# Optimization experiments

Measured on AMD Instinct MI355X. Metric: run time of the kernel, lower is better.

Reference implementation:

```python
import jax, jax.numpy as jnp
import numpy as np

N, L, E, CE = 16384, 50, 64, 128
N_USERS, N_RATINGS, N_CONTENTS = 100000, 6, 50000

def _lin(key, din, dout):
    k1, k2 = jax.random.split(key)
    s = 1.0 / np.sqrt(din)
    return (jax.random.uniform(k1, (din, dout), jnp.float32, -s, s),
            jax.random.uniform(k2, (dout,), jnp.float32, -s, s))

def setup_inputs() -> dict:
    key = jax.random.key(0)
    ks = jax.random.split(key, 16)
    We_w, We_b = _lin(ks[0], CE, E)
    W1_w, W1_b = _lin(ks[1], 2 * E, E)
    W2_w, W2_b = _lin(ks[2], E, E)
    A1_w, A1_b = _lin(ks[3], 2 * E, E)
    A2_w, A2_b = _lin(ks[4], E, E)
    A3_w, A3_b = _lin(ks[5], E, 1)
    Ow_w, Ow_b = _lin(ks[6], 2 * E, E)
    return {
        "u2e": jax.random.normal(ks[7], (N_USERS, E), jnp.float32),
        "r2e": jax.random.normal(ks[8], (N_RATINGS, E), jnp.float32),
        "content_emb": jax.random.normal(ks[9], (N_CONTENTS, CE), jnp.float32),
        "We_w": We_w, "We_b": We_b,
        "W1_w": W1_w, "W1_b": W1_b,
        "W2_w": W2_w, "W2_b": W2_b,
        "A1_w": A1_w, "A1_b": A1_b,
        "A2_w": A2_w, "A2_b": A2_b,
        "A3_w": A3_w, "A3_b": A3_b,
        "Ow_w": Ow_w, "Ow_b": Ow_b,
        "nodes": jnp.arange(N, dtype=jnp.int64) if jax.config.jax_enable_x64 else jnp.arange(N, dtype=jnp.int32),
        "pu_history": jax.random.randint(ks[10], (N, L), 0, N_USERS),
        "pr_history": jax.random.randint(ks[11], (N, L), 0, N_RATINGS),
        "lengths": jax.random.randint(ks[12], (N,), 1, L + 1),
        "pr_content": jax.random.randint(ks[13], (N,), 0, N_CONTENTS),
    }

def reference(u2e, r2e, content_emb, We_w, We_b, W1_w, W1_b, W2_w, W2_b,
              A1_w, A1_b, A2_w, A2_b, A3_w, A3_b, Ow_w, Ow_b,
              nodes, pu_history, pr_history, lengths, pr_content):
    # mask of valid (non-padded) neighbors per node: [N, L]
    mask = jnp.arange(pu_history.shape[1])[None, :] < lengths[:, None]
    # post content representation: [N, E]
    post = jax.nn.relu(content_emb[pr_content] @ We_w + We_b)
    # neighbor embeddings: [N, L, E]
    u = u2e[pu_history]
    r = r2e[pr_history]
    x = jax.nn.relu(jnp.concatenate([u, r], axis=-1) @ W1_w + W1_b)
    o = jax.nn.relu(x @ W2_w + W2_b)  # [N, L, E]
    # attention over variable-length neighbor history
    pr = jnp.broadcast_to(post[:, None, :], o.shape)
    a = jax.nn.relu(jnp.concatenate([o, pr], axis=-1) @ A1_w + A1_b)
    a = jax.nn.relu(a @ A2_w + A2_b)
    logits = (a @ A3_w + A3_b)[..., 0]  # [N, L]
    logits = jnp.where(mask, logits, -jnp.inf)
    att = jax.nn.softmax(logits, axis=1)  # [N, L], padded slots -> 0
    hist = jnp.einsum("nl,nle->ne", att, o)  # [N, E]
    out = jax.nn.relu(jnp.concatenate([hist, post], axis=-1) @ Ow_w + Ow_b)
    return out
```

## Files before the change

### kernel.cpp

```cpp
#include <hip/hip_runtime.h>
#include <hip/hip_bf16.h>
#include <math.h>


#define NN 16384
#define LL 50
#define EE 64
#define NUE 6400000

typedef __attribute__((ext_vector_type(8))) short short8;
typedef __attribute__((ext_vector_type(4))) float f32x4;

#define LGKM_BAR() asm volatile("s_waitcnt lgkmcnt(0)\n\ts_barrier" ::: "memory")

static __device__ __forceinline__ unsigned short f2bf(float x) {
  __hip_bfloat16 h = __float2bfloat16(x);
  unsigned short u;
  __builtin_memcpy(&u, &h, 2);
  return u;
}

static __device__ __forceinline__ float bf2f(unsigned short u) {
  unsigned int v = ((unsigned int)u) << 16;
  float f;
  __builtin_memcpy(&f, &v, 4);
  return f;
}

static __device__ __forceinline__ f32x4 ld4(const float* p) {
  return *(const f32x4*)p;
}

static __device__ __forceinline__ f32x4 relu4(f32x4 a) {
  f32x4 r;
  r[0] = fmaxf(a[0], 0.f); r[1] = fmaxf(a[1], 0.f);
  r[2] = fmaxf(a[2], 0.f); r[3] = fmaxf(a[3], 0.f);
  return r;
}

static __device__ __forceinline__ void gl_lds16(const unsigned short* g,
                                                unsigned char* l) {
  __builtin_amdgcn_global_load_lds(
      (const __attribute__((address_space(1))) void*)g,
      (__attribute__((address_space(3))) void*)l, 16, 0, 0);
}

#define MFMA(A, B, C) __builtin_amdgcn_mfma_f32_16x16x32_bf16((A), (B), (C), 0, 0, 0)
#define SWZ(row, byteoff) ((byteoff) ^ (((row) & 7) << 4))

__global__ __launch_bounds__(1024)
void pre_kernel(const float* __restrict__ u2e, const float* __restrict__ r2e,
                const float* __restrict__ content_emb,
                const int* __restrict__ pr_content,
                const float* __restrict__ We_w, const float* __restrict__ We_b,
                const float* __restrict__ W1_w, const float* __restrict__ W2_w,
                const float* __restrict__ A1_w, const float* __restrict__ A1_b,
                const float* __restrict__ A2_w,
                const int* __restrict__ lengths,
                unsigned short* __restrict__ ur_bf,
                int* __restrict__ buckets, int* __restrict__ wdesc,
                int* __restrict__ Wout, unsigned short* __restrict__ frag_ws,
                float* __restrict__ post_ws, float* __restrict__ abase_ws) {
  const int b = blockIdx.x;
  const int tid = (int)threadIdx.x;
  __shared__ float ce_s[16][128];
  __shared__ float post_s[16][64];
  __shared__ int cnt_s[4];

  if (b == 0) {
    const int lanei = tid & 63;
    if (tid < 4) cnt_s[tid] = 0;
    __syncthreads();
    for (int i0 = 0; i0 < NN; i0 += 1024) {
      const int n = i0 + tid;
      const int ln = lengths[n];
      const int nt = (ln + 15) >> 4;
      const int entry = n | (ln << 14);
#pragma unroll
      for (int bb = 1; bb <= 4; ++bb) {
        const unsigned long long mask = __ballot(nt == bb);
        if (mask) {
          const int leader = __ffsll((long long)mask) - 1;
          int base = 0;
          if (lanei == leader)
            base = atomicAdd(&cnt_s[bb - 1], (int)__popcll(mask));
          base = __shfl(base, leader);
          if (nt == bb) {
            const int rank = __popcll(mask & ((1ull << lanei) - 1ull));
            buckets[(bb - 1) * NN + base + rank] = entry;
          }
        }
      }
    }
    __syncthreads();

    const int c1 = cnt_s[0], c2 = cnt_s[1], c3 = cnt_s[2], c4 = cnt_s[3];
    const int u1 = (c1 < c3) ? c1 : c3;
    const int p2 = c2 >> 1, odd2 = c2 & 1;
    const int rem1 = c1 - u1;
    const int o2ones = odd2 ? ((rem1 < 2) ? rem1 : 2) : 0;
    const int rem1b = rem1 - o2ones;
    const int w4 = c4, w3 = c3, w2 = p2 + odd2, w1 = (rem1b + 3) >> 2;
    const int W = w4 + w3 + w2 + w1;
    if (tid == 0) *Wout = W;

    const int* b1 = buckets;
    const int* b2 = buckets + NN;
    const int* b3 = buckets + 2 * NN;
    const int* b4 = buckets + 3 * NN;
#define ENC(e, t) (((e) & 0x3FFF) | ((t) << 14) | (((e) >> 14) << 16))
    for (int w = tid; w < W; w += 1024) {
      int d0 = -1, d1 = -1, d2 = -1, d3 = -1;
      if (w < w4) {
        const int e = b4[w];
        d0 = ENC(e, 0); d1 = ENC(e, 1); d2 = ENC(e, 2); d3 = ENC(e, 3);
      } else if (w < w4 + w3) {
        const int i = w - w4;
        const int e = b3[i];
        d0 = ENC(e, 0); d1 = ENC(e, 1); d2 = ENC(e, 2);
        if (i < u1) d3 = ENC(b1[i], 0);
      } else if (w < w4 + w3 + w2) {
        const int i = w - w4 - w3;
        if (i < p2) {
          const int ea = b2[2 * i], eb = b2[2 * i + 1];
          d0 = ENC(ea, 0); d1 = ENC(ea, 1); d2 = ENC(eb, 0); d3 = ENC(eb, 1);
        } else {
          const int ea = b2[c2 - 1];
          d0 = ENC(ea, 0); d1 = ENC(ea, 1);
          if (o2ones > 0) d2 = ENC(b1[u1], 0);
          if (o2ones > 1) d3 = ENC(b1[u1 + 1], 0);
        }
      } else {
        const int i = w - w4 - w3 - w2;
        const int basei = u1 + o2ones + 4 * i;
        if (basei + 0 < c1) d0 = ENC(b1[basei + 0], 0);
        if (basei + 1 < c1) d1 = ENC(b1[basei + 1], 0);
        if (basei + 2 < c1) d2 = ENC(b1[basei + 2], 0);
        if (basei + 3 < c1) d3 = ENC(b1[basei + 3], 0);
      }
      int4 v; v.x = d0; v.y = d1; v.z = d2; v.w = d3;
      *(int4*)(wdesc + 4 * w) = v;
    }
#undef ENC
  } else if (b < 1025) {
    const int total8 = (NUE + 384) / 8;
    for (int i = (b - 1) * 1024 + tid; i < total8; i += 1024 * 1024) {
      const long long e0 = (long long)i * 8;
      const float* src = (e0 < NUE) ? (u2e + e0) : (r2e + (e0 - NUE));
      float4 a = *(const float4*)src;
      float4 bb = *(const float4*)(src + 4);
      short8 v;
      v[0] = (short)f2bf(a.x); v[1] = (short)f2bf(a.y);
      v[2] = (short)f2bf(a.z); v[3] = (short)f2bf(a.w);
      v[4] = (short)f2bf(bb.x); v[5] = (short)f2bf(bb.y);
      v[6] = (short)f2bf(bb.z); v[7] = (short)f2bf(bb.w);
      *reinterpret_cast<short8*>(ur_bf + e0) = v;
    }
  } else if (b < 2049) {
    const int sub = tid >> 6;
    const int e = tid & 63;
    const int n = (b - 1025) * 16 + sub;
    const float* ce = content_emb + (size_t)pr_content[n] * 128;
    ce_s[sub][e] = ce[e];
    ce_s[sub][64 + e] = ce[64 + e];
    __syncthreads();
    float acc = We_b[e];
#pragma unroll 8
    for (int k = 0; k < 128; ++k)
      acc = fmaf(ce_s[sub][k], We_w[k * EE + e], acc);
    float po = fmaxf(acc, 0.f);
    post_s[sub][e] = po;
    post_ws[(size_t)n * EE + e] = po;
    __syncthreads();
    float ab = A1_b[e];
#pragma unroll 8
    for (int k = 0; k < 64; ++k)
      ab = fmaf(post_s[sub][k], A1_w[(64 + k) * EE + e], ab);
    abase_ws[(size_t)n * EE + e] = ab;
  } else {
    const int idx = (b - 2049) * 1024 + tid;
    if (idx < 2560) {
      const float* Wm;
      int w, s, lane;
      if (idx < 1024) {
        w = idx >> 8; s = (idx >> 6) & 3; lane = idx & 63; Wm = W1_w;
      } else {
        int r = idx - 1024;
        int li = r >> 9;
        w = (r >> 7) & 3; s = (r >> 6) & 1; lane = r & 63;
        Wm = (li == 0) ? W2_w : (li == 1) ? A1_w : A2_w;
      }
      const int g = lane >> 4, c = lane & 15;
#pragma unroll
      for (int j = 0; j < 8; ++j)
        frag_ws[idx * 8 + j] = f2bf(Wm[(32 * s + 8 * g + j) * EE + 16 * w + c]);
    }
  }
}

__global__
__attribute__((amdgpu_flat_work_group_size(256, 256)))
__attribute__((amdgpu_waves_per_eu(4, 4)))
void fused_kernel(const unsigned short* __restrict__ ur_bf,
                  const float* __restrict__ W1_b, const float* __restrict__ W2_b,
                  const float* __restrict__ A2_b,
                  const float* __restrict__ A3_w, const float* __restrict__ A3_b,
                  const float* __restrict__ Ow_w, const float* __restrict__ Ow_b,
                  const int* __restrict__ pu_history,
                  const int* __restrict__ pr_history,
                  const short8* __restrict__ pf,
                  const float* __restrict__ post_ws,
                  const float* __restrict__ abase_ws,
                  const int* __restrict__ wdesc, const int* __restrict__ Wptr,
                  float* __restrict__ out) {
  const int tid = (int)threadIdx.x;
  const int lane = tid & 63;
  const int w = tid >> 6;
  const int g = lane >> 4;
  const int c = lane & 15;

  __shared__ __align__(16) unsigned char xb0[16384];
  __shared__ __align__(16) unsigned char xb1[8192];
  __shared__ __align__(16) unsigned char xb2[8192];
  __shared__ float bias_s[256];
  __shared__ float lpart[4][64];
  __shared__ float att_s[64];
  __shared__ float h_s[4][128];

  short8 Wf1[4], Wf2[2], Wf3[2], Wf4[2];
#pragma unroll
  for (int s = 0; s < 4; ++s) Wf1[s] = pf[(w * 4 + s) * 64 + lane];
#pragma unroll
  for (int s = 0; s < 2; ++s) {
    Wf2[s] = pf[1024 + (w * 2 + s) * 64 + lane];
    Wf3[s] = pf[1536 + (w * 2 + s) * 64 + lane];
    Wf4[s] = pf[2048 + (w * 2 + s) * 64 + lane];
  }
  if (tid < 64) {
    bias_s[tid]       = W1_b[tid];
    bias_s[64 + tid]  = W2_b[tid];
    bias_s[128 + tid] = A2_b[tid];
    bias_s[192 + tid] = A3_w[tid];
  }

  const float b3 = A3_b[0];
  const float owb = Ow_b[lane];
  const unsigned short* rbase = ur_bf + NUE;
  const int Wtot = *Wptr;
  const int stride = gridDim.x;

  const int r0 = lane >> 4;
  const int cE = (lane & 15) ^ r0;
  const int cO = (lane & 15) ^ (r0 + 4);
  const unsigned short* tabE = ((cE < 8) ? ur_bf : rbase) + (cE & 7) * 8;
  const unsigned short* tabO = ((cO < 8) ? ur_bf : rbase) + (cO & 7) * 8;
  const int* histE = (cE < 8) ? pu_history : pr_history;
  const int* histO = (cO < 8) ? pu_history : pr_history;
  unsigned char* const sbase = xb0 + w * 4096;

  if (blockIdx.x < Wtot) {
    const int dn = wdesc[blockIdx.x * 4 + w];
    if (dn >= 0) {
      const int nd = (dn & 0x3FFF) * LL + (((dn >> 14) & 3) << 4);
      const int lim = ((dn >> 16) & 63) - (((dn >> 14) & 3) << 4);
#pragma unroll
      for (int b = 0; b < 4; ++b) {
        const int row = b * 4 + r0;
        const int* hh = (b & 1) ? histO : histE;
        const unsigned short* tt = (b & 1) ? tabO : tabE;
        if (row < lim) {
          const int idx = hh[nd + row];
          gl_lds16(tt + (size_t)idx * EE, sbase + b * 1024);
        }
      }
    }
  }
  __syncthreads();

  for (int wi = blockIdx.x; wi < Wtot; wi += stride) {
    const int d0 = wdesc[wi * 4 + 0];
    const int d1 = wdesc[wi * 4 + 1];
    const int d2 = wdesc[wi * 4 + 2];
    const int d3 = wdesc[wi * 4 + 3];
    const int dw = (w == 0) ? d0 : (w == 1) ? d1 : (w == 2) ? d2 : d3;
    const bool fin = (dw >= 0) && (((dw >> 14) & 3) == 0);
    const int fnode = dw & 0x3FFF;
    const int flen = (dw >> 16) & 63;

    float po = 0.f;
    if (fin) po = post_ws[(size_t)fnode * EE + lane];

    const int win = wi + stride;
    int sidx0 = 0, sidx1 = 0, sidx2 = 0, sidx3 = 0;
    int svmask = 0;
    if (win < Wtot) {
      const int dn = wdesc[win * 4 + w];
      if (dn >= 0) {
        const int nd = (dn & 0x3FFF) * LL + (((dn >> 14) & 3) << 4);
        const int lim = ((dn >> 16) & 63) - (((dn >> 14) & 3) << 4);
        if (r0 + 0  < lim) { sidx0 = histE[nd + r0];      svmask |= 1; }
        if (r0 + 4  < lim) { sidx1 = histO[nd + r0 + 4];  svmask |= 2; }
        if (r0 + 8  < lim) { sidx2 = histE[nd + r0 + 8];  svmask |= 4; }
        if (r0 + 12 < lim) { sidx3 = histO[nd + r0 + 12]; svmask |= 8; }
      }
    }

    f32x4 acc[4];

    {
      const f32x4 binit = ld4(bias_s + 16 * w + 4 * g);
#pragma unroll
      for (int rt = 0; rt < 4; ++rt) acc[rt] = binit;
#pragma unroll
      for (int s = 0; s < 4; ++s)
#pragma unroll
        for (int rt = 0; rt < 4; ++rt) {
          const int row = rt * 16 + c;
          const short8 bf =
              *(const short8*)(xb0 + SWZ(row, row * 256 + s * 64 + g * 16));
          acc[rt] = MFMA(Wf1[s], bf, acc[rt]);
        }
#pragma unroll
      for (int rt = 0; rt < 4; ++rt) {
        const f32x4 v = relu4(acc[rt]);
        ushort4 p;
        p.x = f2bf(v[0]); p.y = f2bf(v[1]); p.z = f2bf(v[2]); p.w = f2bf(v[3]);
        const int row = rt * 16 + c;
        *(ushort4*)(xb1 + SWZ(row, row * 128 + w * 32 + g * 8)) = p;
      }
    }
    LGKM_BAR();

    if (svmask & 1) gl_lds16(tabE + (size_t)sidx0 * EE, sbase);
    if (svmask & 2) gl_lds16(tabO + (size_t)sidx1 * EE, sbase + 1024);
    if (svmask & 4) gl_lds16(tabE + (size_t)sidx2 * EE, sbase + 2048);
    if (svmask & 8) gl_lds16(tabO + (size_t)sidx3 * EE, sbase + 3072);

    {
      const f32x4 binit = ld4(bias_s + 64 + 16 * w + 4 * g);
#pragma unroll
      for (int rt = 0; rt < 4; ++rt) acc[rt] = binit;
#pragma unroll
      for (int s = 0; s < 2; ++s)
#pragma unroll
        for (int rt = 0; rt < 4; ++rt) {
          const int row = rt * 16 + c;
          const short8 bf =
              *(const short8*)(xb1 + SWZ(row, row * 128 + s * 64 + g * 16));
          acc[rt] = MFMA(Wf2[s], bf, acc[rt]);
        }
#pragma unroll
      for (int rt = 0; rt < 4; ++rt) {
        const f32x4 v = relu4(acc[rt]);
        ushort4 p;
        p.x = f2bf(v[0]); p.y = f2bf(v[1]); p.z = f2bf(v[2]); p.w = f2bf(v[3]);
        const int row = rt * 16 + c;
        *(ushort4*)(xb2 + SWZ(row, row * 128 + w * 32 + g * 8)) = p;
      }
    }
    LGKM_BAR();

    {
      {
        const int n0 = (d0 >= 0) ? (d0 & 0x3FFF) : 0;
        const int n1 = (d1 >= 0) ? (d1 & 0x3FFF) : 0;
        const int n2 = (d2 >= 0) ? (d2 & 0x3FFF) : 0;
        const int n3 = (d3 >= 0) ? (d3 & 0x3FFF) : 0;
        acc[0] = ld4(abase_ws + (size_t)n0 * EE + 16 * w + 4 * g);
        acc[1] = ld4(abase_ws + (size_t)n1 * EE + 16 * w + 4 * g);
        acc[2] = ld4(abase_ws + (size_t)n2 * EE + 16 * w + 4 * g);
        acc[3] = ld4(abase_ws + (size_t)n3 * EE + 16 * w + 4 * g);
      }
#pragma unroll
      for (int s = 0; s < 2; ++s)
#pragma unroll
        for (int rt = 0; rt < 4; ++rt) {
          const int row = rt * 16 + c;
          const short8 bf =
              *(const short8*)(xb2 + SWZ(row, row * 128 + s * 64 + g * 16));
          acc[rt] = MFMA(Wf3[s], bf, acc[rt]);
        }
#pragma unroll
      for (int rt = 0; rt < 4; ++rt) {
        const f32x4 v = relu4(acc[rt]);
        ushort4 p;
        p.x = f2bf(v[0]); p.y = f2bf(v[1]); p.z = f2bf(v[2]); p.w = f2bf(v[3]);
        const int row = rt * 16 + c;
        *(ushort4*)(xb1 + SWZ(row, row * 128 + w * 32 + g * 8)) = p;
      }
    }
    LGKM_BAR();

    {
      const f32x4 binit = ld4(bias_s + 128 + 16 * w + 4 * g);
#pragma unroll
      for (int rt = 0; rt < 4; ++rt) acc[rt] = binit;
#pragma unroll
      for (int s = 0; s < 2; ++s)
#pragma unroll
        for (int rt = 0; rt < 4; ++rt) {
          const int row = rt * 16 + c;
          const short8 bf =
              *(const short8*)(xb1 + SWZ(row, row * 128 + s * 64 + g * 16));
          acc[rt] = MFMA(Wf4[s], bf, acc[rt]);
        }
      const f32x4 a3 = ld4(bias_s + 192 + 16 * w + 4 * g);
#pragma unroll
      for (int rt = 0; rt < 4; ++rt) {
        const f32x4 r = relu4(acc[rt]);
        float p = r[0] * a3[0];
        p = fmaf(r[1], a3[1], p);
        p = fmaf(r[2], a3[2], p);
        p = fmaf(r[3], a3[3], p);
        p += __shfl_xor(p, 16);
        p += __shfl_xor(p, 32);
        if (lane < 16) lpart[w][rt * 16 + lane] = p;
      }
    }
    __syncthreads();

    if (fin) {
      const bool vr = (lane < flen);
      float lg = -INFINITY;
      if (vr) {
        const int row = w * 16 + lane;
        lg = lpart[0][row] + lpart[1][row] + lpart[2][row] + lpart[3][row] + b3;
      }
      float mx = lg;
#pragma unroll
      for (int off = 32; off > 0; off >>= 1)
        mx = fmaxf(mx, __shfl_xor(mx, off));
      const float e = __expf(lg - mx);
      float sm = e;
#pragma unroll
      for (int off = 32; off > 0; off >>= 1) sm += __shfl_xor(sm, off);
      if (vr) att_s[w * 16 + lane] = e / sm;

      float h0 = 0.f, h1 = 0.f;
      for (int r2 = 0; r2 + 1 < flen; r2 += 2) {
        const int ra = w * 16 + r2, rb = ra + 1;
        const unsigned short oa =
            *(const unsigned short*)(xb2 + SWZ(ra, ra * 128 + lane * 2));
        const unsigned short ob =
            *(const unsigned short*)(xb2 + SWZ(rb, rb * 128 + lane * 2));
        h0 = fmaf(att_s[ra], bf2f(oa), h0);
        h1 = fmaf(att_s[rb], bf2f(ob), h1);
      }
      if (flen & 1) {
        const int ra = w * 16 + flen - 1;
        const unsigned short oa =
            *(const unsigned short*)(xb2 + SWZ(ra, ra * 128 + lane * 2));
        h0 = fmaf(att_s[ra], bf2f(oa), h0);
      }
      h_s[w][lane] = h0 + h1;
      h_s[w][64 + lane] = po;

      float s0 = 0.f, s1 = 0.f, s2 = 0.f, s3 = 0.f;
#pragma unroll 8
      for (int k = 0; k < 128; k += 4) {
        s0 = fmaf(h_s[w][k],     Ow_w[(k)     * EE + lane], s0);
        s1 = fmaf(h_s[w][k + 1], Ow_w[(k + 1) * EE + lane], s1);
        s2 = fmaf(h_s[w][k + 2], Ow_w[(k + 2) * EE + lane], s2);
        s3 = fmaf(h_s[w][k + 3], Ow_w[(k + 3) * EE + lane], s3);
      }
      const float a = owb + ((s0 + s1) + (s2 + s3));
      out[(size_t)fnode * EE + lane] = fmaxf(a, 0.f);
    }
  }
}

template <int K>
__device__ __forceinline__ void mm2(const float* row0, const float* row1,
                                    const float* __restrict__ W, int e,
                                    float& acc0, float& acc1) {
  const float4* r0 = (const float4*)row0;
  const float4* r1 = (const float4*)row1;
#pragma unroll 4
  for (int k4 = 0; k4 < K / 4; ++k4) {
    float4 va = r0[k4];
    float4 vb = r1[k4];
    const float* w = W + (k4 * 4) * EE + e;
    float w0 = w[0], w1 = w[EE], w2 = w[2 * EE], w3 = w[3 * EE];
    acc0 = fmaf(va.x, w0, acc0);  acc1 = fmaf(vb.x, w0, acc1);
    acc0 = fmaf(va.y, w1, acc0);  acc1 = fmaf(vb.y, w1, acc1);
    acc0 = fmaf(va.z, w2, acc0);  acc1 = fmaf(vb.z, w2, acc1);
    acc0 = fmaf(va.w, w3, acc0);  acc1 = fmaf(vb.w, w3, acc1);
  }
}

__global__ __launch_bounds__(256, 4)
void postenc_kernel(
    const float* __restrict__ u2e, const float* __restrict__ r2e,
    const float* __restrict__ content_emb,
    const float* __restrict__ We_w, const float* __restrict__ We_b,
    const float* __restrict__ W1_w, const float* __restrict__ W1_b,
    const float* __restrict__ W2_w, const float* __restrict__ W2_b,
    const float* __restrict__ A1_w, const float* __restrict__ A1_b,
    const float* __restrict__ A2_w, const float* __restrict__ A2_b,
    const float* __restrict__ A3_w, const float* __restrict__ A3_b,
    const float* __restrict__ Ow_w, const float* __restrict__ Ow_b,
    const int* __restrict__ pu_history, const int* __restrict__ pr_history,
    const int* __restrict__ lengths, const int* __restrict__ pr_content,
    float* __restrict__ out) {
  const int n = blockIdx.x;
  const int tid = (int)threadIdx.x;
  const int e = tid & 63;
  const int g = tid >> 6;

  __shared__ float post_s[EE];
  __shared__ float abase_s[EE];
  __shared__ float in_s[8][128];
  __shared__ float x_s[8][EE];
  __shared__ float a_s[8][EE];
  __shared__ float o_s[56][EE];
  __shared__ float logit_s[EE];
  __shared__ float att_s[EE];
  __shared__ float red_s[4][EE];

  const int len = lengths[n];
  float p = 0.f;

  if (g == 0) {
    const float* ce = content_emb + (size_t)pr_content[n] * 128;
    float acc = We_b[e];
#pragma unroll 4
    for (int k = 0; k < 128; ++k) acc = fmaf(ce[k], We_w[k * EE + e], acc);
    p = fmaxf(acc, 0.f);
    post_s[e] = p;
    float ab = A1_b[e];
#pragma unroll
    for (int k = 0; k < 64; ++k) {
      float pk = __shfl(p, k);
      ab = fmaf(pk, A1_w[(64 + k) * EE + e], ab);
    }
    abase_s[e] = ab;
    logit_s[e] = -INFINITY;
  }
  __syncthreads();

  for (int lb = 0; lb < 56; lb += 8) {
    const int l0 = lb + g;
    const int l1 = l0 + 4;
    const bool v0 = l0 < LL;
    const bool v1 = l1 < LL;

    int pu0 = 0, pr0 = 0, pu1 = 0, pr1 = 0;
    if (v0) { pu0 = pu_history[n * LL + l0]; pr0 = pr_history[n * LL + l0]; }
    if (v1) { pu1 = pu_history[n * LL + l1]; pr1 = pr_history[n * LL + l1]; }
    in_s[g][e]          = v0 ? u2e[(size_t)pu0 * EE + e] : 0.f;
    in_s[g][64 + e]     = v0 ? r2e[pr0 * EE + e]         : 0.f;
    in_s[g + 4][e]      = v1 ? u2e[(size_t)pu1 * EE + e] : 0.f;
    in_s[g + 4][64 + e] = v1 ? r2e[pr1 * EE + e]         : 0.f;
    __syncthreads();

    float acc0 = W1_b[e], acc1 = acc0;
    mm2<128>(in_s[g], in_s[g + 4], W1_w, e, acc0, acc1);
    x_s[g][e]     = fmaxf(acc0, 0.f);
    x_s[g + 4][e] = fmaxf(acc1, 0.f);
    __syncthreads();

    acc0 = W2_b[e]; acc1 = acc0;
    mm2<64>(x_s[g], x_s[g + 4], W2_w, e, acc0, acc1);
    float o0 = fmaxf(acc0, 0.f);
    float o1 = fmaxf(acc1, 0.f);
    if (v0) o_s[l0][e] = o0;
    if (v1) o_s[l1][e] = o1;
    x_s[g][e]     = o0;
    x_s[g + 4][e] = o1;
    __syncthreads();

    acc0 = abase_s[e]; acc1 = acc0;
    mm2<64>(x_s[g], x_s[g + 4], A1_w, e, acc0, acc1);
    a_s[g][e]     = fmaxf(acc0, 0.f);
    a_s[g + 4][e] = fmaxf(acc1, 0.f);
    __syncthreads();

    acc0 = A2_b[e]; acc1 = acc0;
    mm2<64>(a_s[g], a_s[g + 4], A2_w, e, acc0, acc1);
    float w3 = A3_w[e];
    float p0 = fmaxf(acc0, 0.f) * w3;
    float p1 = fmaxf(acc1, 0.f) * w3;
#pragma unroll
    for (int off = 32; off > 0; off >>= 1) {
      p0 += __shfl_xor(p0, off);
      p1 += __shfl_xor(p1, off);
    }
    if (e == 0) {
      float b3 = A3_b[0];
      if (l0 < len) logit_s[l0] = p0 + b3;
      if (l1 < len) logit_s[l1] = p1 + b3;
    }
    __syncthreads();
  }

  if (g == 0) {
    float lg = logit_s[e];
    float m = lg;
#pragma unroll
    for (int off = 32; off > 0; off >>= 1) m = fmaxf(m, __shfl_xor(m, off));
    float pe = __expf(lg - m);
    float sm = pe;
#pragma unroll
    for (int off = 32; off > 0; off >>= 1) sm += __shfl_xor(sm, off);
    att_s[e] = pe / sm;
  }
  __syncthreads();

  {
    const int l_lo = 13 * g;
    const int l_hi = (13 * g + 13 < LL) ? 13 * g + 13 : LL;
    float h = 0.f;
    for (int l = l_lo; l < l_hi; ++l) h = fmaf(att_s[l], o_s[l][e], h);
    red_s[g][e] = h;
  }
  __syncthreads();

  if (g == 0) {
    float h = red_s[0][e] + red_s[1][e] + red_s[2][e] + red_s[3][e];
    float acc = Ow_b[e];
#pragma unroll
    for (int k = 0; k < 64; ++k) {
      float hk = __shfl(h, k);
      acc = fmaf(hk, Ow_w[k * EE + e], acc);
    }
#pragma unroll
    for (int k = 0; k < 64; ++k) {
      float pk = __shfl(p, k);
      acc = fmaf(pk, Ow_w[(64 + k) * EE + e], acc);
    }
    out[(size_t)n * EE + e] = fmaxf(acc, 0.f);
  }
}

extern "C" void kernel_launch(void* const* d_in, const int* in_sizes, int n_in,
                              void* d_out, int out_size, void* d_ws, size_t ws_size,
                              hipStream_t stream) {
  const float* u2e         = (const float*)d_in[0];
  const float* r2e         = (const float*)d_in[1];
  const float* content_emb = (const float*)d_in[2];
  const float* We_w = (const float*)d_in[3];
  const float* We_b = (const float*)d_in[4];
  const float* W1_w = (const float*)d_in[5];
  const float* W1_b = (const float*)d_in[6];
  const float* W2_w = (const float*)d_in[7];
  const float* W2_b = (const float*)d_in[8];
  const float* A1_w = (const float*)d_in[9];
  const float* A1_b = (const float*)d_in[10];
  const float* A2_w = (const float*)d_in[11];
  const float* A2_b = (const float*)d_in[12];
  const float* A3_w = (const float*)d_in[13];
  const float* A3_b = (const float*)d_in[14];
  const float* Ow_w = (const float*)d_in[15];
  const float* Ow_b = (const float*)d_in[16];
  const int* pu_history = (const int*)d_in[18];
  const int* pr_history = (const int*)d_in[19];
  const int* lengths    = (const int*)d_in[20];
  const int* pr_content = (const int*)d_in[21];
  float* out = (float*)d_out;

  const size_t FR_OFF  = 0;
  const size_t PO_OFF  = 65536;
  const size_t AB_OFF  = PO_OFF + (size_t)NN * EE * 4;
  const size_t UBF_OFF = AB_OFF + (size_t)NN * EE * 4;
  const size_t CNT_OFF = UBF_OFF + (size_t)(NUE + 384) * 2;
  const size_t BK_OFF  = CNT_OFF + 256;
  const size_t WD_OFF  = BK_OFF + (size_t)4 * NN * 4;
  const size_t NEED    = WD_OFF + (size_t)NN * 4 * 4;

  if (ws_size < NEED) {
    postenc_kernel<<<NN, 256, 0, stream>>>(
        u2e, r2e, content_emb, We_w, We_b, W1_w, W1_b, W2_w, W2_b,
        A1_w, A1_b, A2_w, A2_b, A3_w, A3_b, Ow_w, Ow_b,
        pu_history, pr_history, lengths, pr_content, out);
    return;
  }

  char* wsp = (char*)d_ws;
  unsigned short* frag_ws = (unsigned short*)(wsp + FR_OFF);
  float* post_ws  = (float*)(wsp + PO_OFF);
  float* abase_ws = (float*)(wsp + AB_OFF);
  unsigned short* ur_bf = (unsigned short*)(wsp + UBF_OFF);
  int* Wout_ws = (int*)(wsp + CNT_OFF);
  int* bk_ws   = (int*)(wsp + BK_OFF);
  int* wd_ws   = (int*)(wsp + WD_OFF);

  pre_kernel<<<2052, 1024, 0, stream>>>(
      u2e, r2e, content_emb, pr_content, We_w, We_b, W1_w, W2_w,
      A1_w, A1_b, A2_w, lengths, ur_bf, bk_ws, wd_ws, Wout_ws,
      frag_ws, post_ws, abase_ws);
  fused_kernel<<<1024, 256, 0, stream>>>(
      ur_bf, W1_b, W2_b, A2_b, A3_w, A3_b, Ow_w, Ow_b,
      pu_history, pr_history, (const short8*)frag_ws,
      post_ws, abase_ws, wd_ws, Wout_ws, out);
}
```

Measured before the change: 132.0 us.

## Replace static grid-stride work distribution with atomic work-stealing counter

New measurement: 163.4 us. 1.24x slower.

```diff
diff --git a/kernel.cpp b/kernel.cpp
--- a/kernel.cpp
+++ b/kernel.cpp
@@ -7,6 +7,7 @@
 #define LL 50
 #define EE 64
 #define NUE 6400000
+#define FGRID 1024
 
 typedef __attribute__((ext_vector_type(8))) short short8;
 typedef __attribute__((ext_vector_type(4))) float f32x4;
@@ -59,7 +60,8 @@
                 const int* __restrict__ lengths,
                 unsigned short* __restrict__ ur_bf,
                 int* __restrict__ buckets, int* __restrict__ wdesc,
-                int* __restrict__ Wout, unsigned short* __restrict__ frag_ws,
+                int* __restrict__ Wout, int* __restrict__ wctr,
+                unsigned short* __restrict__ frag_ws,
                 float* __restrict__ post_ws, float* __restrict__ abase_ws) {
   const int b = blockIdx.x;
   const int tid = (int)threadIdx.x;
@@ -70,6 +72,7 @@
   if (b == 0) {
     const int lanei = tid & 63;
     if (tid < 4) cnt_s[tid] = 0;
+    if (tid == 8) *wctr = FGRID;
     __syncthreads();
     for (int i0 = 0; i0 < NN; i0 += 1024) {
       const int n = i0 + tid;
@@ -212,6 +215,7 @@
                   const float* __restrict__ post_ws,
                   const float* __restrict__ abase_ws,
                   const int* __restrict__ wdesc, const int* __restrict__ Wptr,
+                  int* __restrict__ wctr,
                   float* __restrict__ out) {
   const int tid = (int)threadIdx.x;
   const int lane = tid & 63;
@@ -226,6 +230,7 @@
   __shared__ float lpart[4][64];
   __shared__ float att_s[64];
   __shared__ float h_s[4][128];
+  __shared__ int nxt_s;
 
   short8 Wf1[4], Wf2[2], Wf3[2], Wf4[2];
 #pragma unroll
@@ -247,7 +252,6 @@
   const float owb = Ow_b[lane];
   const unsigned short* rbase = ur_bf + NUE;
   const int Wtot = *Wptr;
-  const int stride = gridDim.x;
 
   const int r0 = lane >> 4;
   const int cE = (lane & 15) ^ r0;
@@ -258,8 +262,9 @@
   const int* histO = (cO < 8) ? pu_history : pr_history;
   unsigned char* const sbase = xb0 + w * 4096;
 
-  if (blockIdx.x < Wtot) {
-    const int dn = wdesc[blockIdx.x * 4 + w];
+  int wi = blockIdx.x;
+  if (wi < Wtot) {
+    const int dn = wdesc[wi * 4 + w];
     if (dn >= 0) {
       const int nd = (dn & 0x3FFF) * LL + (((dn >> 14) & 3) << 4);
       const int lim = ((dn >> 16) & 63) - (((dn >> 14) & 3) << 4);
@@ -277,7 +282,9 @@
   }
   __syncthreads();
 
-  for (int wi = blockIdx.x; wi < Wtot; wi += stride) {
+  while (wi < Wtot) {
+    if (tid == 0) nxt_s = atomicAdd(wctr, 1);
+
     const int d0 = wdesc[wi * 4 + 0];
     const int d1 = wdesc[wi * 4 + 1];
     const int d2 = wdesc[wi * 4 + 2];
@@ -290,21 +297,6 @@
     float po = 0.f;
     if (fin) po = post_ws[(size_t)fnode * EE + lane];
 
-    const int win = wi + stride;
-    int sidx0 = 0, sidx1 = 0, sidx2 = 0, sidx3 = 0;
-    int svmask = 0;
-    if (win < Wtot) {
-      const int dn = wdesc[win * 4 + w];
-      if (dn >= 0) {
-        const int nd = (dn & 0x3FFF) * LL + (((dn >> 14) & 3) << 4);
-        const int lim = ((dn >> 16) & 63) - (((dn >> 14) & 3) << 4);
-        if (r0 + 0  < lim) { sidx0 = histE[nd + r0];      svmask |= 1; }
-        if (r0 + 4  < lim) { sidx1 = histO[nd + r0 + 4];  svmask |= 2; }
-        if (r0 + 8  < lim) { sidx2 = histE[nd + r0 + 8];  svmask |= 4; }
-        if (r0 + 12 < lim) { sidx3 = histO[nd + r0 + 12]; svmask |= 8; }
-      }
-    }
-
     f32x4 acc[4];
 
     {
@@ -331,10 +323,22 @@
     }
     LGKM_BAR();
 
-    if (svmask & 1) gl_lds16(tabE + (size_t)sidx0 * EE, sbase);
-    if (svmask & 2) gl_lds16(tabO + (size_t)sidx1 * EE, sbase + 1024);
-    if (svmask & 4) gl_lds16(tabE + (size_t)sidx2 * EE, sbase + 2048);
-    if (svmask & 8) gl_lds16(tabO + (size_t)sidx3 * EE, sbase + 3072);
+    const int win = nxt_s;
+    if (win < Wtot) {
+      const int dn = wdesc[win * 4 + w];
+      if (dn >= 0) {
+        const int nd = (dn & 0x3FFF) * LL + (((dn >> 14) & 3) << 4);
+        const int lim = ((dn >> 16) & 63) - (((dn >> 14) & 3) << 4);
+        if (r0 + 0 < lim)
+          gl_lds16(tabE + (size_t)histE[nd + r0] * EE, sbase);
+        if (r0 + 4 < lim)
+          gl_lds16(tabO + (size_t)histO[nd + r0 + 4] * EE, sbase + 1024);
+        if (r0 + 8 < lim)
+          gl_lds16(tabE + (size_t)histE[nd + r0 + 8] * EE, sbase + 2048);
+        if (r0 + 12 < lim)
+          gl_lds16(tabO + (size_t)histO[nd + r0 + 12] * EE, sbase + 3072);
+      }
+    }
 
     {
       const f32x4 binit = ld4(bias_s + 64 + 16 * w + 4 * g);
@@ -466,6 +470,7 @@
       const float a = owb + ((s0 + s1) + (s2 + s3));
       out[(size_t)fnode * EE + lane] = fmaxf(a, 0.f);
     }
+    wi = win;
   }
 }
 
@@ -681,15 +686,16 @@
   float* abase_ws = (float*)(wsp + AB_OFF);
   unsigned short* ur_bf = (unsigned short*)(wsp + UBF_OFF);
   int* Wout_ws = (int*)(wsp + CNT_OFF);
+  int* wctr_ws = Wout_ws + 16;
   int* bk_ws   = (int*)(wsp + BK_OFF);
   int* wd_ws   = (int*)(wsp + WD_OFF);
 
   pre_kernel<<<2052, 1024, 0, stream>>>(
       u2e, r2e, content_emb, pr_content, We_w, We_b, W1_w, W2_w,
-      A1_w, A1_b, A2_w, lengths, ur_bf, bk_ws, wd_ws, Wout_ws,
+      A1_w, A1_b, A2_w, lengths, ur_bf, bk_ws, wd_ws, Wout_ws, wctr_ws,
       frag_ws, post_ws, abase_ws);
-  fused_kernel<<<1024, 256, 0, stream>>>(
+  fused_kernel<<<FGRID, 256, 0, stream>>>(
       ur_bf, W1_b, W2_b, A2_b, A3_w, A3_b, Ow_w, Ow_b,
       pu_history, pr_history, (const short8*)frag_ws,
-      post_ws, abase_ws, wd_ws, Wout_ws, out);
-}
+      post_ws, abase_ws, wd_ws, Wout_ws, wctr_ws, out);
+}
```
